# Kernel optimization log

Measured on AMD Instinct MI355X. Metric: run time of the kernel, lower is better.

The kernel has to match this reference:

```python
import jax, jax.numpy as jnp
import numpy as np

B, S, D, H = 8, 1024, 1024, 16
HD = D // H  # 64


def setup_inputs() -> dict:
    key = jax.random.key(0)
    ks = jax.random.split(key, 10)
    f32 = jnp.float32
    inp = {
        "query": jax.random.normal(ks[0], (B, S, D), f32),
        "key": jax.random.normal(ks[1], (B, S, D), f32),
        "value": jax.random.normal(ks[2], (B, S, D), f32),
        "rel": jax.random.normal(ks[3], (B, S, S), f32),
        "timestamp": jax.random.normal(ks[4], (B, S, S), f32),
        "mask": jax.random.randint(ks[5], (B, S, S), 0, 2).astype(bool),
        "l1": jnp.float32(0.3),
        "l2": jnp.float32(0.5),
        "encode_pos": 0,
        "Wq": jax.random.normal(ks[6], (D, D), f32) * 0.02,
        "bq": jnp.zeros((D,), f32),
        "Wk": jax.random.normal(ks[7], (D, D), f32) * 0.02,
        "bk": jnp.zeros((D,), f32),
        "Wv": jax.random.normal(ks[8], (D, D), f32) * 0.02,
        "bv": jnp.zeros((D,), f32),
    }
    return inp


def _proj(x, W, b):
    # nn.Linear: x @ W.T + b, then split heads -> [B, H, S, HD]
    y = x @ W.T + b
    return y.reshape(B, S, H, HD).transpose(0, 2, 1, 3)


def reference(query, key, value, rel, timestamp, mask, l1, l2, encode_pos,
              Wq, bq, Wk, bk, Wv, bv):
    # encode_pos == 0 path: QK^T + time-decay + rel-attn three-softmax blend
    q = _proj(query, Wq, bq)
    k = _proj(key, Wk, bk)
    v = _proj(value, Wv, bv)

    m = mask[:, None]                       # [B,1,S,S], broadcasts over heads
    mf = m.astype(jnp.float32)

    # rel attention: zero out where mask is False, then fill zeros with -1e5
    rel_m = rel[:, None] * mf               # [B,1,S,S]
    rel_attn = jax.nn.softmax(jnp.where(rel_m == 0, -100000.0, rel_m), axis=-1)

    inv_sqrt_d = 1.0 / np.sqrt(HD).astype(np.float32)
    scores = jnp.einsum("bhqd,bhkd->bhqk", q, k) * inv_sqrt_d
    scores = jnp.where(m, -1e32, scores)

    time_stamp = jnp.exp(-jnp.abs(timestamp[:, None]))   # [B,1,S,S]
    time_stamp = jnp.where(m, -100000.0, time_stamp)

    prob_attn = jax.nn.softmax(scores, axis=-1)          # [B,H,S,S]
    time_attn = jax.nn.softmax(time_stamp, axis=-1)      # [B,1,S,S]

    prob_attn = (1.0 - l2) * prob_attn + l2 * time_attn
    prob_attn = (1.0 - l1) * prob_attn + l1 * rel_attn
    # dropout is identity at inference

    out = jnp.einsum("bhqk,bhkd->bhqd", prob_attn, v)
    out = out.transpose(0, 2, 1, 3).reshape(B, S, D)
    return out, prob_attn
```

## Files before the change

### kernel.cpp

```cpp
#include <hip/hip_runtime.h>
#include <hip/hip_fp16.h>
#include <stdint.h>

typedef short bf16x8 __attribute__((ext_vector_type(8)));
typedef short bf16x4 __attribute__((ext_vector_type(4)));
typedef float f32x4 __attribute__((ext_vector_type(4)));
typedef unsigned short u16x4 __attribute__((ext_vector_type(4)));
typedef unsigned short u16x8 __attribute__((ext_vector_type(8)));

constexpr int NB = 8, NS = 1024, ND = 1024, NH = 16, NHD = 64;

static __device__ __forceinline__ unsigned short f2bf(float f) {
    union { float f; uint32_t u; } v; v.f = f;
    uint32_t r = (v.u + 0x7fffu + ((v.u >> 16) & 1u)) >> 16;
    return (unsigned short)r;
}

static __device__ __forceinline__ unsigned short f2h(float f) {
    return __half_as_ushort(__float2half(f));
}
static __device__ __forceinline__ float h2f(unsigned short h) {
    return __half2float(__ushort_as_half(h));
}

static __device__ __forceinline__ f32x4 mfma32(bf16x8 a, bf16x8 b, f32x4 c) {
    return __builtin_amdgcn_mfma_f32_16x16x32_bf16(a, b, c, 0, 0, 0);
}

static __device__ __forceinline__ f32x4 mfma16(bf16x4 a, bf16x4 b, f32x4 c) {
#if __has_builtin(__builtin_amdgcn_mfma_f32_16x16x16bf16_1k)
    return __builtin_amdgcn_mfma_f32_16x16x16bf16_1k(a, b, c, 0, 0, 0);
#elif __has_builtin(__builtin_amdgcn_mfma_f32_16x16x16_bf16)
    return __builtin_amdgcn_mfma_f32_16x16x16_bf16(a, b, c, 0, 0, 0);
#else
    asm volatile("v_mfma_f32_16x16x16_bf16 %0, %1, %2, %0\n\ts_nop 7\n\ts_nop 7"
                 : "+v"(c) : "v"(a), "v"(b));
    return c;
#endif
}

static __device__ __forceinline__ bool mask_at(const void* m, size_t idx, int ms) {
    if (ms == 4) return ((const unsigned int*)m)[idx] != 0u;
    return ((const unsigned char*)m)[idx] != 0;
}

__global__ void detect_mask(const unsigned int* __restrict__ m, int* __restrict__ flag) {
    int l = threadIdx.x;
    bool bad = false;
    for (int i = l; i < 1024; i += 64) {
        unsigned int w = m[i];
        bad |= (w > 1u && w != 0x3f800000u);
    }
    bad = (bool)__any(bad);
    if (l == 0) *flag = bad ? 1 : 4;
}

__global__ __launch_bounds__(256) void cvt_frag(const float* __restrict__ in,
                                                unsigned short* __restrict__ out, int nunits) {
    int nw = (gridDim.x * blockDim.x) >> 6;
    int w = (blockIdx.x * blockDim.x + threadIdx.x) >> 6;
    int l = threadIdx.x & 63;
    int mr = l & 15, sub = l >> 4;
    for (int u = w; u < nunits; u += nw) {
        int mg = u >> 5, kt = u & 31;
        const float4* p = (const float4*)(in + ((size_t)(mg * 16 + mr)) * 1024 + kt * 32 + sub * 8);
        float4 a = p[0], b = p[1];
        u16x8 o;
        o[0] = f2bf(a.x); o[1] = f2bf(a.y); o[2] = f2bf(a.z); o[3] = f2bf(a.w);
        o[4] = f2bf(b.x); o[5] = f2bf(b.y); o[6] = f2bf(b.z); o[7] = f2bf(b.w);
        *(u16x8*)(out + ((size_t)u * 64 + l) * 8) = o;
    }
}

__global__ __launch_bounds__(256) void proj_gemm(const unsigned short* __restrict__ Af,
                                                 const unsigned short* __restrict__ Wf,
                                                 const float* __restrict__ bias,
                                                 unsigned short* __restrict__ C, int mode) {
    int l = threadIdx.x & 63, w = threadIdx.x >> 6;
    int lr = l & 15, lg = l >> 4;
    int m_base = blockIdx.y * 128 + (w >> 1) * 64;
    int n_base = blockIdx.x * 128 + (w & 1) * 64;
    int mtg0 = m_base >> 4, ntg0 = n_base >> 4;
    f32x4 acc[4][4] = {};
    for (int kt = 0; kt < 32; kt++) {
        bf16x8 af[4], bfr[4];
        #pragma unroll
        for (int mt = 0; mt < 4; mt++)
            af[mt] = *(const bf16x8*)(Af + (((size_t)(mtg0 + mt) * 32 + kt) * 64 + l) * 8);
        #pragma unroll
        for (int nt = 0; nt < 4; nt++)
            bfr[nt] = *(const bf16x8*)(Wf + (((size_t)(ntg0 + nt) * 32 + kt) * 64 + l) * 8);
        #pragma unroll
        for (int mt = 0; mt < 4; mt++) {
            #pragma unroll
            for (int nt = 0; nt < 4; nt++)
                acc[mt][nt] = mfma32(af[mt], bfr[nt], acc[mt][nt]);
        }
    }
    #pragma unroll
    for (int mt = 0; mt < 4; mt++) {
        #pragma unroll
        for (int nt = 0; nt < 4; nt++) {
            int col = n_base + nt * 16 + lr;
            int row0 = m_base + mt * 16 + lg * 4;
            float bv = bias[col];
            int b = row0 >> 10;
            int h = col >> 6;
            if (mode == 0) {
                int st = (row0 & 1023) >> 4;
                int d32 = (col & 63) >> 5;
                int sub = (col & 31) >> 3;
                int e = col & 7;
                size_t base = ((((size_t)(b * NH + h) * 64 + st) * 2 + d32) * 64) * 8;
                #pragma unroll
                for (int r = 0; r < 4; r++) {
                    int lane = lg * 4 + r + 16 * sub;
                    C[base + (size_t)lane * 8 + e] = f2bf(acc[mt][nt][r] + bv);
                }
            } else {
                int s0 = row0 & 1023;
                int tg = s0 >> 4;
                int tp = tg >> 1, half = tg & 1;
                int dd = col & 63;
                int dt = dd >> 4;
                int lane = (dd & 15) + 16 * lg;
                u16x4 pk;
                #pragma unroll
                for (int r = 0; r < 4; r++) pk[r] = f2bf(acc[mt][nt][r] + bv);
                size_t addr = ((((size_t)(b * NH + h) * 32 + tp) * 4 + dt) * 64 + lane) * 8
                              + half * 4;
                *(u16x4*)(C + addr) = pk;
            }
        }
    }
}

__global__ __launch_bounds__(256) void tr_kernel(const float* __restrict__ rel,
                                                 const float* __restrict__ ts,
                                                 const void* __restrict__ maskp,
                                                 const int* __restrict__ msflag,
                                                 const float* __restrict__ l1p,
                                                 const float* __restrict__ l2p,
                                                 unsigned short* __restrict__ TRh,
                                                 uint32_t* __restrict__ PMf) {
    __shared__ float s_tm[4], s_rm[4], s_ts[4], s_rs[4];
    __shared__ unsigned char s_nib[256];
    int row = blockIdx.x;
    int t = threadIdx.x, w = t >> 6, l = t & 63;
    int ms = *msflag;
    size_t base = (size_t)row * NS;
    float4 r4 = ((const float4*)(rel + base))[t];
    float4 t4 = ((const float4*)(ts + base))[t];
    float rr[4], tt[4];
    *(float4*)rr = r4; *(float4*)tt = t4;
    float tv[4], rv[4];
    unsigned nib = 0;
    float tmx = -3.0e38f, rmx = -3.0e38f;
    #pragma unroll
    for (int j = 0; j < 4; j++) {
        bool m = mask_at(maskp, base + t * 4 + j, ms);
        nib |= (m ? 1u : 0u) << j;
        tv[j] = m ? -100000.0f : __expf(-fabsf(tt[j]));
        float rm_ = m ? rr[j] : 0.0f;
        rv[j] = (rm_ == 0.0f) ? -100000.0f : rm_;
        tmx = fmaxf(tmx, tv[j]); rmx = fmaxf(rmx, rv[j]);
    }
    s_nib[t] = (unsigned char)nib;
    #pragma unroll
    for (int off = 1; off < 64; off <<= 1) {
        tmx = fmaxf(tmx, __shfl_xor(tmx, off));
        rmx = fmaxf(rmx, __shfl_xor(rmx, off));
    }
    if (l == 0) { s_tm[w] = tmx; s_rm[w] = rmx; }
    __syncthreads();
    tmx = fmaxf(fmaxf(s_tm[0], s_tm[1]), fmaxf(s_tm[2], s_tm[3]));
    rmx = fmaxf(fmaxf(s_rm[0], s_rm[1]), fmaxf(s_rm[2], s_rm[3]));
    float te[4], re[4], tsum = 0.f, rsum = 0.f;
    #pragma unroll
    for (int j = 0; j < 4; j++) {
        te[j] = __expf(tv[j] - tmx); tsum += te[j];
        re[j] = __expf(rv[j] - rmx); rsum += re[j];
    }
    #pragma unroll
    for (int off = 1; off < 64; off <<= 1) {
        tsum += __shfl_xor(tsum, off);
        rsum += __shfl_xor(rsum, off);
    }
    if (l == 0) { s_ts[w] = tsum; s_rs[w] = rsum; }
    __syncthreads();
    tsum = s_ts[0] + s_ts[1] + s_ts[2] + s_ts[3];
    rsum = s_rs[0] + s_rs[1] + s_rs[2] + s_rs[3];
    float l1 = *l1p, l2 = *l2p;
    float ti = ((1.0f - l1) * l2) / tsum;
    float ri = l1 / rsum;
    u16x4 oh;
    oh[0] = f2h(te[0] * ti + re[0] * ri);
    oh[1] = f2h(te[1] * ti + re[1] * ri);
    oh[2] = f2h(te[2] * ti + re[2] * ri);
    oh[3] = f2h(te[3] * ti + re[3] * ri);
    int b = row >> 10, q = row & 1023;
    int qt = q >> 4, qr = q & 15;
    size_t slot = ((size_t)(b * 64 + qt) * 64 + (t >> 2)) * 64 + (qr + 16 * (t & 3));
    ((u16x4*)TRh)[slot] = oh;
    if (t < 32) {
        uint32_t word = 0;
        #pragma unroll
        for (int i = 0; i < 8; i++)
            word |= ((uint32_t)s_nib[t * 8 + i]) << (i * 4);
        PMf[((size_t)(b * 64 + qt) * 16 + qr) * 32 + t] = word;
    }
}

__global__ __launch_bounds__(64, 4) void att_pv_kernel(const unsigned short* __restrict__ Qf,
                                                       const unsigned short* __restrict__ Kf,
                                                       const uint32_t* __restrict__ PMf,
                                                       const unsigned short* __restrict__ TRh,
                                                       const float* __restrict__ l1p,
                                                       const float* __restrict__ l2p,
                                                       const unsigned short* __restrict__ Vf,
                                                       float* __restrict__ probOut,
                                                       float* __restrict__ outp) {
    int bid = blockIdx.x;
    int swz = ((bid & 7) << 10) | (bid >> 3);
    int qt = swz & 63;
    int h = (swz >> 6) & 15;
    int b = swz >> 10;
    int l = threadIdx.x, lr = l & 15, lg = l >> 4;
    int q0 = qt * 16;
    int q = q0 + lr;
    size_t bh = (size_t)(b * NH + h);

    const unsigned short* qf = Qf + (((bh * 64 + qt) * 2) * 64 + l) * 8;
    bf16x8 bq0 = *(const bf16x8*)(qf);
    bf16x8 bq1 = *(const bf16x8*)(qf + 64 * 8);

    const unsigned short* kfb = Kf + ((bh * 64 * 2) * 64) * 8 + (size_t)l * 8;
    const uint32_t* pmrow = PMf + ((size_t)(b * 64 + qt) * 16 + lr) * 32;

    float sm = 0.f;
    for (int t8 = 0; t8 < 8; t8++) {
        uint32_t pmw[4];
        *(uint4*)pmw = *(const uint4*)(pmrow + t8 * 4);
        #pragma unroll
        for (int tt = 0; tt < 8; tt++) {
            int t = t8 * 8 + tt;
            const unsigned short* kp = kfb + (size_t)t * 1024;
            bf16x8 a0 = *(const bf16x8*)kp;
            bf16x8 a1 = *(const bf16x8*)(kp + 512);
            f32x4 acc = {};
            acc = mfma32(a0, bq0, acc);
            acc = mfma32(a1, bq1, acc);
            uint32_t word = pmw[tt >> 1];
            int shift = (tt & 1) * 16 + lg * 4;
            #pragma unroll
            for (int r = 0; r < 4; r++) {
                bool m = (word >> (shift + r)) & 1u;
                sm += m ? 0.0f : __expf(acc[r] * 0.125f);
            }
        }
    }
    sm += __shfl_xor(sm, 16);
    sm += __shfl_xor(sm, 32);
    float l1 = *l1p, l2 = *l2p;
    float rinv = ((1.0f - l1) * (1.0f - l2)) / sm;

    float* po = probOut + bh * NS * NS + (size_t)q * NS;
    const u16x4* trh = (const u16x4*)TRh + ((size_t)(b * 64 + qt) * 64) * 64 + l;
    const unsigned short* vf = Vf + (bh * 32 * 4 * 64) * 8 + (size_t)l * 8;
    f32x4 acc2[4] = {};
    for (int tq = 0; tq < 8; tq++) {
        uint32_t pmw[4];
        *(uint4*)pmw = *(const uint4*)(pmrow + tq * 4);
        #pragma unroll
        for (int tpi = 0; tpi < 4; tpi++) {
            int tp = tq * 4 + tpi;
            bf16x4 pf0, pf1;
            #pragma unroll
            for (int hf = 0; hf < 2; hf++) {
                int t = tp * 2 + hf;
                const unsigned short* kp = kfb + (size_t)t * 1024;
                bf16x8 a0 = *(const bf16x8*)kp;
                bf16x8 a1 = *(const bf16x8*)(kp + 512);
                f32x4 acc = {};
                acc = mfma32(a0, bq0, acc);
                acc = mfma32(a1, bq1, acc);
                uint32_t word = pmw[tpi];
                int shift = hf * 16 + lg * 4;
                u16x4 tr4 = trh[(size_t)t * 64];
                float4 o;
                float e0 = ((word >> (shift + 0)) & 1u) ? 0.f : __expf(acc[0] * 0.125f);
                float e1 = ((word >> (shift + 1)) & 1u) ? 0.f : __expf(acc[1] * 0.125f);
                float e2 = ((word >> (shift + 2)) & 1u) ? 0.f : __expf(acc[2] * 0.125f);
                float e3 = ((word >> (shift + 3)) & 1u) ? 0.f : __expf(acc[3] * 0.125f);
                o.x = e0 * rinv + h2f(tr4[0]);
                o.y = e1 * rinv + h2f(tr4[1]);
                o.z = e2 * rinv + h2f(tr4[2]);
                o.w = e3 * rinv + h2f(tr4[3]);
                *(float4*)(po + t * 16 + lg * 4) = o;
                bf16x4 pk;
                pk[0] = (short)f2bf(o.x); pk[1] = (short)f2bf(o.y);
                pk[2] = (short)f2bf(o.z); pk[3] = (short)f2bf(o.w);
                if (hf == 0) pf0 = pk; else pf1 = pk;
            }
            #pragma unroll
            for (int dt = 0; dt < 4; dt++) {
                bf16x8 vv = *(const bf16x8*)(vf + (size_t)(tp * 4 + dt) * 512);
                bf16x4 v0 = __builtin_shufflevector(vv, vv, 0, 1, 2, 3);
                bf16x4 v1 = __builtin_shufflevector(vv, vv, 4, 5, 6, 7);
                acc2[dt] = mfma16(v0, pf0, acc2[dt]);
                acc2[dt] = mfma16(v1, pf1, acc2[dt]);
            }
        }
    }
    float* orow = outp + ((size_t)b * NS + q) * ND + h * NHD + lg * 4;
    #pragma unroll
    for (int dt = 0; dt < 4; dt++) {
        float4 ov;
        ov.x = acc2[dt][0]; ov.y = acc2[dt][1]; ov.z = acc2[dt][2]; ov.w = acc2[dt][3];
        *(float4*)(orow + dt * 16) = ov;
    }
}

extern "C" void kernel_launch(void* const* d_in, const int* in_sizes, int n_in,
                              void* d_out, int out_size, void* d_ws, size_t ws_size,
                              hipStream_t stream) {
    const float* query = (const float*)d_in[0];
    const float* key   = (const float*)d_in[1];
    const float* value = (const float*)d_in[2];
    const float* rel   = (const float*)d_in[3];
    const float* ts    = (const float*)d_in[4];
    const void*  mask  = d_in[5];
    const float* l1p   = (const float*)d_in[6];
    const float* l2p   = (const float*)d_in[7];
    const float* Wq = (const float*)d_in[9];
    const float* bq = (const float*)d_in[10];
    const float* Wk = (const float*)d_in[11];
    const float* bk = (const float*)d_in[12];
    const float* Wv = (const float*)d_in[13];
    const float* bv = (const float*)d_in[14];

    char* ws = (char*)d_ws;
    const size_t SZ = (size_t)NB * NS * ND * 2;
    unsigned short* Qf  = (unsigned short*)(ws);
    unsigned short* Kf  = (unsigned short*)(ws + SZ);
    unsigned short* Vf  = (unsigned short*)(ws + 2 * SZ);
    unsigned short* Afq = (unsigned short*)(ws + 3 * SZ);
    unsigned short* Afk = (unsigned short*)(ws + 4 * SZ);
    unsigned short* Afv = (unsigned short*)(ws + 5 * SZ);
    unsigned short* Wfq = (unsigned short*)(ws + 6 * SZ);
    unsigned short* Wfk = (unsigned short*)(ws + 6 * SZ + 2u * 1024 * 1024);
    unsigned short* Wfv = (unsigned short*)(ws + 6 * SZ + 4u * 1024 * 1024);
    int* msflag         = (int*)(ws + 6 * SZ + 6u * 1024 * 1024);
    uint32_t* PMf       = (uint32_t*)(ws + 6 * SZ + 8u * 1024 * 1024);
    unsigned short* TRh = (unsigned short*)(ws + 3 * SZ);

    detect_mask<<<1, 64, 0, stream>>>((const unsigned int*)mask, msflag);

    const int nuX = NB * NS * 2;
    const int nuW = 1024 * 2;
    cvt_frag<<<512, 256, 0, stream>>>(query, Afq, nuX);
    cvt_frag<<<512, 256, 0, stream>>>(key,   Afk, nuX);
    cvt_frag<<<512, 256, 0, stream>>>(value, Afv, nuX);
    cvt_frag<<<128, 256, 0, stream>>>(Wq, Wfq, nuW);
    cvt_frag<<<128, 256, 0, stream>>>(Wk, Wfk, nuW);
    cvt_frag<<<128, 256, 0, stream>>>(Wv, Wfv, nuW);

    dim3 pg(8, 64);
    proj_gemm<<<pg, 256, 0, stream>>>(Afq, Wfq, bq, Qf, 0);
    proj_gemm<<<pg, 256, 0, stream>>>(Afk, Wfk, bk, Kf, 0);
    proj_gemm<<<pg, 256, 0, stream>>>(Afv, Wfv, bv, Vf, 1);

    tr_kernel<<<NB * NS, 256, 0, stream>>>(rel, ts, mask, msflag, l1p, l2p, TRh, PMf);

    float* outp = (float*)d_out;
    float* probOut = outp + (size_t)NB * NS * ND;
    att_pv_kernel<<<NB * NH * (NS / 16), 64, 0, stream>>>(Qf, Kf, PMf, TRh, l1p, l2p, Vf,
                                                          probOut, outp);
}
```

Measured before the change: 514.1 us.

## Fuse fp32-to-bf16 conversion into projection GEMM loads and split softmax-sum accumulators

```diff
diff --git a/kernel.cpp b/kernel.cpp
--- a/kernel.cpp
+++ b/kernel.cpp
@@ -39,6 +39,17 @@
 #endif
 }
 
+static __device__ __forceinline__ bf16x8 ld_cvt8(const float* p) {
+    float4 a = *(const float4*)p;
+    float4 b = *(const float4*)(p + 4);
+    bf16x8 o;
+    o[0] = (short)f2bf(a.x); o[1] = (short)f2bf(a.y);
+    o[2] = (short)f2bf(a.z); o[3] = (short)f2bf(a.w);
+    o[4] = (short)f2bf(b.x); o[5] = (short)f2bf(b.y);
+    o[6] = (short)f2bf(b.z); o[7] = (short)f2bf(b.w);
+    return o;
+}
+
 static __device__ __forceinline__ bool mask_at(const void* m, size_t idx, int ms) {
     if (ms == 4) return ((const unsigned int*)m)[idx] != 0u;
     return ((const unsigned char*)m)[idx] != 0;
@@ -55,41 +66,24 @@
     if (l == 0) *flag = bad ? 1 : 4;
 }
 
-__global__ __launch_bounds__(256) void cvt_frag(const float* __restrict__ in,
-                                                unsigned short* __restrict__ out, int nunits) {
-    int nw = (gridDim.x * blockDim.x) >> 6;
-    int w = (blockIdx.x * blockDim.x + threadIdx.x) >> 6;
-    int l = threadIdx.x & 63;
-    int mr = l & 15, sub = l >> 4;
-    for (int u = w; u < nunits; u += nw) {
-        int mg = u >> 5, kt = u & 31;
-        const float4* p = (const float4*)(in + ((size_t)(mg * 16 + mr)) * 1024 + kt * 32 + sub * 8);
-        float4 a = p[0], b = p[1];
-        u16x8 o;
-        o[0] = f2bf(a.x); o[1] = f2bf(a.y); o[2] = f2bf(a.z); o[3] = f2bf(a.w);
-        o[4] = f2bf(b.x); o[5] = f2bf(b.y); o[6] = f2bf(b.z); o[7] = f2bf(b.w);
-        *(u16x8*)(out + ((size_t)u * 64 + l) * 8) = o;
-    }
-}
-
-__global__ __launch_bounds__(256) void proj_gemm(const unsigned short* __restrict__ Af,
-                                                 const unsigned short* __restrict__ Wf,
+__global__ __launch_bounds__(256) void proj_gemm(const float* __restrict__ A,
+                                                 const float* __restrict__ W,
                                                  const float* __restrict__ bias,
                                                  unsigned short* __restrict__ C, int mode) {
     int l = threadIdx.x & 63, w = threadIdx.x >> 6;
     int lr = l & 15, lg = l >> 4;
     int m_base = blockIdx.y * 128 + (w >> 1) * 64;
     int n_base = blockIdx.x * 128 + (w & 1) * 64;
-    int mtg0 = m_base >> 4, ntg0 = n_base >> 4;
     f32x4 acc[4][4] = {};
     for (int kt = 0; kt < 32; kt++) {
+        int kc = kt * 32 + lg * 8;
         bf16x8 af[4], bfr[4];
         #pragma unroll
         for (int mt = 0; mt < 4; mt++)
-            af[mt] = *(const bf16x8*)(Af + (((size_t)(mtg0 + mt) * 32 + kt) * 64 + l) * 8);
+            af[mt] = ld_cvt8(A + (size_t)(m_base + mt * 16 + lr) * 1024 + kc);
         #pragma unroll
         for (int nt = 0; nt < 4; nt++)
-            bfr[nt] = *(const bf16x8*)(Wf + (((size_t)(ntg0 + nt) * 32 + kt) * 64 + l) * 8);
+            bfr[nt] = ld_cvt8(W + (size_t)(n_base + nt * 16 + lr) * 1024 + kc);
         #pragma unroll
         for (int mt = 0; mt < 4; mt++) {
             #pragma unroll
@@ -237,7 +231,7 @@
     const unsigned short* kfb = Kf + ((bh * 64 * 2) * 64) * 8 + (size_t)l * 8;
     const uint32_t* pmrow = PMf + ((size_t)(b * 64 + qt) * 16 + lr) * 32;
 
-    float sm = 0.f;
+    float sma[4] = {0.f, 0.f, 0.f, 0.f};
     for (int t8 = 0; t8 < 8; t8++) {
         uint32_t pmw[4];
         *(uint4*)pmw = *(const uint4*)(pmrow + t8 * 4);
@@ -255,10 +249,11 @@
             #pragma unroll
             for (int r = 0; r < 4; r++) {
                 bool m = (word >> (shift + r)) & 1u;
-                sm += m ? 0.0f : __expf(acc[r] * 0.125f);
+                sma[r] += m ? 0.0f : __expf(acc[r] * 0.125f);
             }
         }
     }
+    float sm = (sma[0] + sma[1]) + (sma[2] + sma[3]);
     sm += __shfl_xor(sm, 16);
     sm += __shfl_xor(sm, 32);
     float l1 = *l1p, l2 = *l2p;
@@ -344,31 +339,16 @@
     unsigned short* Qf  = (unsigned short*)(ws);
     unsigned short* Kf  = (unsigned short*)(ws + SZ);
     unsigned short* Vf  = (unsigned short*)(ws + 2 * SZ);
-    unsigned short* Afq = (unsigned short*)(ws + 3 * SZ);
-    unsigned short* Afk = (unsigned short*)(ws + 4 * SZ);
-    unsigned short* Afv = (unsigned short*)(ws + 5 * SZ);
-    unsigned short* Wfq = (unsigned short*)(ws + 6 * SZ);
-    unsigned short* Wfk = (unsigned short*)(ws + 6 * SZ + 2u * 1024 * 1024);
-    unsigned short* Wfv = (unsigned short*)(ws + 6 * SZ + 4u * 1024 * 1024);
-    int* msflag         = (int*)(ws + 6 * SZ + 6u * 1024 * 1024);
-    uint32_t* PMf       = (uint32_t*)(ws + 6 * SZ + 8u * 1024 * 1024);
     unsigned short* TRh = (unsigned short*)(ws + 3 * SZ);
+    int* msflag         = (int*)(ws + 4 * SZ);
+    uint32_t* PMf       = (uint32_t*)(ws + 4 * SZ + 1024u * 1024);
 
     detect_mask<<<1, 64, 0, stream>>>((const unsigned int*)mask, msflag);
 
-    const int nuX = NB * NS * 2;
-    const int nuW = 1024 * 2;
-    cvt_frag<<<512, 256, 0, stream>>>(query, Afq, nuX);
-    cvt_frag<<<512, 256, 0, stream>>>(key,   Afk, nuX);
-    cvt_frag<<<512, 256, 0, stream>>>(value, Afv, nuX);
-    cvt_frag<<<128, 256, 0, stream>>>(Wq, Wfq, nuW);
-    cvt_frag<<<128, 256, 0, stream>>>(Wk, Wfk, nuW);
-    cvt_frag<<<128, 256, 0, stream>>>(Wv, Wfv, nuW);
-
     dim3 pg(8, 64);
-    proj_gemm<<<pg, 256, 0, stream>>>(Afq, Wfq, bq, Qf, 0);
-    proj_gemm<<<pg, 256, 0, stream>>>(Afk, Wfk, bk, Kf, 0);
-    proj_gemm<<<pg, 256, 0, stream>>>(Afv, Wfv, bv, Vf, 1);
+    proj_gemm<<<pg, 256, 0, stream>>>(query, Wq, bq, Qf, 0);
+    proj_gemm<<<pg, 256, 0, stream>>>(key,   Wk, bk, Kf, 0);
+    proj_gemm<<<pg, 256, 0, stream>>>(value, Wv, bv, Vf, 1);
 
     tr_kernel<<<NB * NS, 256, 0, stream>>>(rel, ts, mask, msflag, l1p, l2p, TRh, PMf);
 
```

Result: slower. 779.1 us (+51.5%).
